# Kernel tuning notes

Hardware: AMD Instinct MI355X
Metric: run time of the kernel (lower is better)

## Reference

```python
import jax, jax.numpy as jnp
import numpy as np


def _resize_bilinear(x, h, w):
    # matches F.upsample(mode='bilinear', align_corners=False) (half-pixel centers)
    return jax.image.resize(x, (x.shape[0], x.shape[1], h, w), method='bilinear')


def _build_volume_2d(fl, fr, maxdisp):
    # fl, fr: [B,C,H,W] -> cost [B,D,H,W], D=maxdisp (stride=1)
    B, C, H, W = fl.shape
    d = jnp.arange(maxdisp)
    src = jnp.arange(W)[None, :] - d[:, None]          # [D,W]
    valid = (src >= 0).astype(fl.dtype)
    src_c = jnp.clip(src, 0, W - 1)
    fr_sh = fr[:, :, :, src_c] * valid                  # [B,C,H,D,W]; zeros where w<d
    cost = jnp.abs(fl[:, :, :, None, :] - fr_sh).sum(axis=1)  # [B,H,D,W]
    return jnp.transpose(cost, (0, 2, 1, 3))            # [B,D,H,W]


def _warp(fr, disp):
    # fr: [B,C,H,W]; disp: [B,K,H,W] horizontal disparity (sample at x - disp)
    # bilinear along W, zero padding (grid_sample semantics, align_corners=True grid)
    B, C, H, W = fr.shape
    xs = jnp.arange(W, dtype=fr.dtype)[None, None, None, :] - disp   # [B,K,H,W]
    x0 = jnp.floor(xs)
    w1 = xs - x0                                        # frac weight for right neighbor
    x0i = x0.astype(jnp.int32)
    x1i = x0i + 1
    v0 = ((x0i >= 0) & (x0i < W)).astype(fr.dtype)
    v1 = ((x1i >= 0) & (x1i < W)).astype(fr.dtype)
    x0c = jnp.clip(x0i, 0, W - 1)
    x1c = jnp.clip(x1i, 0, W - 1)

    def gather(idx):  # idx [B,K,H,W] -> [B,K,C,H,W]
        idxb = jnp.broadcast_to(idx[:, :, None, :, :], (B, idx.shape[1], C, H, W))
        return jnp.take_along_axis(fr[:, None], idxb, axis=-1)

    g0 = gather(x0c) * v0[:, :, None]
    g1 = gather(x1c) * v1[:, :, None]
    return g0 * (1.0 - w1)[:, :, None] + g1 * w1[:, :, None]   # [B,K,C,H,W]


def _build_volume_2d3(fl, fr, maxdisp, disp):
    # fl, fr: [B,C,H,W]; disp: [B,1,H,W] coarse disparity. K = 2*maxdisp-1 shifts.
    shifts = jnp.arange(-maxdisp + 1, maxdisp, dtype=fl.dtype)       # [K]
    bd = disp - shifts[None, :, None, None]                          # [B,K,H,W]
    warped = _warp(fr, bd)                                           # [B,K,C,H,W]
    return jnp.abs(fl[:, None] - warped).sum(axis=2)                 # [B,K,H,W]


def _regress(cost, start, end):
    # softmax(-cost) over disparity axis, weighted sum with disp values [start,end)
    p = jax.nn.softmax(-cost, axis=1)
    dvals = jnp.arange(start, end, dtype=cost.dtype)[None, :, None, None]
    return jnp.sum(p * dvals, axis=1, keepdims=True)                 # [B,1,H,W]


def setup_inputs() -> dict:
    key = jax.random.key(0)
    k = jax.random.split(key, 4)
    return {
        "feat_l0": jax.random.normal(k[0], (4, 32, 64, 128), dtype=jnp.float32),
        "feat_r0": jax.random.normal(k[1], (4, 32, 64, 128), dtype=jnp.float32),
        "feat_l1": jax.random.normal(k[2], (4, 32, 128, 256), dtype=jnp.float32),
        "feat_r1": jax.random.normal(k[3], (4, 32, 128, 256), dtype=jnp.float32),
        "img_h": 512,
        "img_w": 1024,
        "maxdisp0": 12,
        "maxdisp1": 3,
    }


def reference(feat_l0, feat_r0, feat_l1, feat_r1, img_h, img_w, maxdisp0, maxdisp1):
    H0 = feat_l0.shape[2]
    H1, W1 = feat_l1.shape[2], feat_l1.shape[3]

    cost0 = _build_volume_2d(feat_l0, feat_r0, maxdisp0)             # [B,D0,H0,W0]
    pred_low0 = _regress(cost0, 0, maxdisp0) * (img_h / H0)
    pred0 = _resize_bilinear(pred_low0, img_h, img_w)                # [B,1,img_h,img_w]

    # ---- scale 1: residual cost volume via warp around coarse disparity ----
    wflow = _resize_bilinear(pred0, H1, W1) * (H1 / img_h)           # [B,1,H1,W1]
    cost1 = _build_volume_2d3(feat_l1, feat_r1, maxdisp1, wflow)     # [B,2*D1-1,H1,W1]
    pred_low1 = _regress(cost1, -maxdisp1 + 1, maxdisp1) * (img_h / H1)
    pred1 = _resize_bilinear(pred_low1, img_h, img_w) + pred0

    return (pred0, pred1)
```

## Files before the change

### kernel.cpp

```cpp
#include <hip/hip_runtime.h>

#define NB 4
#define NC 32
#define H0 64
#define W0 128
#define D0 12
#define H1 128
#define W1 256
#define NK 5
#define IMH 512
#define IMW 1024

#define S0L 144
#define G0L 16
#define S1L 288
#define G1L 28

typedef __attribute__((address_space(3))) uint32_t as3_u32;
typedef const __attribute__((address_space(1))) uint32_t as1_u32;

__global__ __launch_bounds__(512) void k_main(
        const float* __restrict__ fl0, const float* __restrict__ fr0,
        const float* __restrict__ fl1, const float* __restrict__ fr1,
        float* __restrict__ pl0, float* __restrict__ pl1) {
    const int bk = blockIdx.x;
    const int b = bk >> 6, m = bk & 63;
    const int tid = threadIdx.x;
    const int wave = tid >> 6, lane = tid & 63;

    __shared__ float frs1[2][NC][S1L];
    __shared__ float frs0[3][NC][S0L];
    __shared__ float p0l[3][W0];
    __shared__ float ytmp[2][W0];
    __shared__ float wfl[2][W1];

#pragma unroll
    for (int j = 0; j < 8; ++j) {
        int idx = wave * 8 + j;
        int it = idx >> 5, c = idx & 31;
        const float* src = fr1 + ((size_t)(b * NC + c) * H1 + (2 * m + it)) * W1
                         + lane * 4;
        as3_u32* dst = (as3_u32*)&frs1[it][c][G1L];
        __builtin_amdgcn_global_load_lds((as1_u32*)src, dst, 16, 0, 0);
    }
    {
        int it = tid >> 8, c = (tid >> 3) & 31, u = tid & 7;
        int col = (u < 7) ? u * 4 : (G1L + W1);
        *(float4*)&frs1[it][c][col] = make_float4(0.f, 0.f, 0.f, 0.f);
    }

#pragma unroll
    for (int i = 0; i < 6; ++i) {
        int idx = i * 512 + tid;
        int rr = idx >> 10, rem = idx & 1023, c = rem >> 5, q = rem & 31;
        int row = min(max(m - 1 + rr, 0), H0 - 1);
        float4 v = *(const float4*)(fr0 + ((size_t)(b * NC + c) * H0 + row) * W0
                                    + q * 4);
        *(float4*)&frs0[rr][c][G0L + q * 4] = v;
    }
    if (tid < 384) {
        int rr = tid >> 7, c = (tid >> 2) & 31, u = tid & 3;
        *(float4*)&frs0[rr][c][u * 4] = make_float4(0.f, 0.f, 0.f, 0.f);
    }

    const int w0g = tid >> 2, g = tid & 3;
    float flv0[3][8];
#pragma unroll
    for (int rr = 0; rr < 3; ++rr) {
        int row = min(max(m - 1 + rr, 0), H0 - 1);
#pragma unroll
        for (int j = 0; j < 8; ++j)
            flv0[rr][j] = fl0[((size_t)(b * NC + 4 * j + g) * H0 + row) * W0 + w0g];
    }
    const int w1 = tid >> 1, hh = tid & 1;
    float flv1[2][16];
#pragma unroll
    for (int it = 0; it < 2; ++it)
#pragma unroll
        for (int j = 0; j < 16; ++j)
            flv1[it][j] = fl1[((size_t)(b * NC + 2 * j + hh) * H1 + 2 * m + it) * W1
                              + w1];
    __syncthreads();

#pragma unroll
    for (int rr = 0; rr < 3; ++rr) {
        float cost[D0];
#pragma unroll
        for (int d = 0; d < D0; ++d) cost[d] = 0.f;
#pragma unroll
        for (int j = 0; j < 8; ++j) {
            const float* sr = &frs0[rr][4 * j + g][G0L + w0g];
            float fv = flv0[rr][j];
#pragma unroll
            for (int d = 0; d < D0; ++d)
                cost[d] += fabsf(fv - sr[-d]);
        }
#pragma unroll
        for (int d = 0; d < D0; ++d) {
            cost[d] += __shfl_xor(cost[d], 1);
            cost[d] += __shfl_xor(cost[d], 2);
        }
        if (g == 0) {
            float mn = cost[0];
#pragma unroll
            for (int d = 1; d < D0; ++d) mn = fminf(mn, cost[d]);
            float s = 0.f, sd = 0.f;
#pragma unroll
            for (int d = 0; d < D0; ++d) {
                float e = expf(mn - cost[d]);
                s += e;
                sd += (float)d * e;
            }
            float val = 8.f * (sd / s);
            p0l[rr][w0g] = val;
            if (rr == 1)
                pl0[((size_t)b * H0 + m) * W0 + w0g] = val;
        }
    }
    __syncthreads();

    if (tid < 256) {
        int it = tid >> 7, col = tid & 127;
        int oy = 2 * m + it;
        float wy0, wy1, wy2;
        if (oy == 0)            { wy0 = 0.f;            wy1 = 27.625f / 28.f; wy2 = 0.375f / 28.f; }
        else if (oy == H1 - 1)  { wy0 = 0.375f / 28.f;  wy1 = 27.625f / 28.f; wy2 = 0.f; }
        else if (oy & 1)        { wy0 = 0.375f / 32.f;  wy1 = 23.25f / 32.f;  wy2 = 8.375f / 32.f; }
        else                    { wy0 = 8.375f / 32.f;  wy1 = 23.25f / 32.f;  wy2 = 0.375f / 32.f; }
        ytmp[it][col] = wy0 * p0l[0][col] + wy1 * p0l[1][col] + wy2 * p0l[2][col];
    }
    __syncthreads();
    {
        int it = tid >> 8, ox = tid & 255;
        int n = ox >> 1;
        int c0, c1, c2;
        float wx0, wx1, wx2;
        if (ox == 0) {
            c0 = 0; c1 = 0; c2 = 1;
            wx0 = 0.f; wx1 = 27.625f / 28.f; wx2 = 0.375f / 28.f;
        } else if (ox == W1 - 1) {
            c0 = W0 - 2; c1 = W0 - 1; c2 = W0 - 1;
            wx0 = 0.375f / 28.f; wx1 = 27.625f / 28.f; wx2 = 0.f;
        } else {
            c0 = max(n - 1, 0); c1 = n; c2 = min(n + 1, W0 - 1);
            if (ox & 1) { wx0 = 0.375f / 32.f; wx1 = 23.25f / 32.f; wx2 = 8.375f / 32.f; }
            else        { wx0 = 8.375f / 32.f; wx1 = 23.25f / 32.f; wx2 = 0.375f / 32.f; }
        }
        wfl[it][ox] = 0.25f * (wx0 * ytmp[it][c0] + wx1 * ytmp[it][c1]
                             + wx2 * ytmp[it][c2]);
    }
    __syncthreads();

#pragma unroll
    for (int it = 0; it < 2; ++it) {
        float disp = wfl[it][w1];
        float xs = (float)w1 - disp;
        float xbf = floorf(xs);
        float f = xs - xbf;
        int xb = (int)xbf;
        const float* sr = &frs1[it][0][G1L + xb - 2];

        float cost[NK];
#pragma unroll
        for (int k = 0; k < NK; ++k) cost[k] = 0.f;
#pragma unroll
        for (int j = 0; j < 16; ++j) {
            const float* row = sr + (2 * j + hh) * S1L;
            float g0 = row[0], g1 = row[1], g2 = row[2];
            float g3 = row[3], g4 = row[4], g5 = row[5];
            float fv = flv1[it][j];
            cost[0] += fabsf(fv - (g0 + f * (g1 - g0)));
            cost[1] += fabsf(fv - (g1 + f * (g2 - g1)));
            cost[2] += fabsf(fv - (g2 + f * (g3 - g2)));
            cost[3] += fabsf(fv - (g3 + f * (g4 - g3)));
            cost[4] += fabsf(fv - (g5 * f + g4 * (1.f - f)));
        }
#pragma unroll
        for (int k = 0; k < NK; ++k) cost[k] += __shfl_xor(cost[k], 1);
        if (hh == 0) {
            float mn = cost[0];
#pragma unroll
            for (int k = 1; k < NK; ++k) mn = fminf(mn, cost[k]);
            float s = 0.f, sd = 0.f;
#pragma unroll
            for (int k = 0; k < NK; ++k) {
                float e = expf(mn - cost[k]);
                s += e;
                sd += (float)(k - 2) * e;
            }
            pl1[((size_t)b * H1 + 2 * m + it) * W1 + w1] = 4.f * (sd / s);
        }
    }
}

__global__ __launch_bounds__(256, 4) void k_final(const float* __restrict__ pl0,
                                                  const float* __restrict__ pl1,
                                                  float* __restrict__ out) {
    const int blk = blockIdx.x;
    const int b = blk >> 9, y = blk & (IMH - 1);
    const int tid = threadIdx.x;
    __shared__ float a0[W0];
    __shared__ float a1[W1];

    const float* p0b = pl0 + (size_t)b * H0 * W0;
    const float* p1b = pl1 + (size_t)b * H1 * W1;

    float sy0 = (y + 0.5f) * 0.125f - 0.5f;
    float y0f = floorf(sy0);
    float fy0 = sy0 - y0f;
    int r0 = (int)y0f;
    int r0c = min(max(r0, 0), H0 - 1), r1c = min(max(r0 + 1, 0), H0 - 1);

    float sy1 = (y + 0.5f) * 0.25f - 0.5f;
    float y1f = floorf(sy1);
    float fy1 = sy1 - y1f;
    int s0 = (int)y1f;
    int s0c = min(max(s0, 0), H1 - 1), s1c = min(max(s0 + 1, 0), H1 - 1);

    if (tid < W0) {
        float u = p0b[r0c * W0 + tid], v = p0b[r1c * W0 + tid];
        a0[tid] = u + fy0 * (v - u);
    }
    {
        float u = p1b[s0c * W1 + tid], v = p1b[s1c * W1 + tid];
        a1[tid] = u + fy1 * (v - u);
    }
    __syncthreads();

    float v0[4], v1[4];
#pragma unroll
    for (int i = 0; i < 4; ++i) {
        int x = tid * 4 + i;
        float sx0 = (x + 0.5f) * 0.125f - 0.5f;
        float x0f = floorf(sx0);
        float fx0 = sx0 - x0f;
        int c0 = (int)x0f;
        int c0c = min(max(c0, 0), W0 - 1), c1c = min(max(c0 + 1, 0), W0 - 1);
        float p0 = a0[c0c] + fx0 * (a0[c1c] - a0[c0c]);

        float sx1 = (x + 0.5f) * 0.25f - 0.5f;
        float x1f = floorf(sx1);
        float fx1 = sx1 - x1f;
        int d0 = (int)x1f;
        int d0c = min(max(d0, 0), W1 - 1), d1c = min(max(d0 + 1, 0), W1 - 1);
        float p1 = a1[d0c] + fx1 * (a1[d1c] - a1[d0c]);

        v0[i] = p0;
        v1[i] = p1 + p0;
    }
    const size_t NPXQ = (size_t)NB * IMH * IMW / 4;
    size_t t = (size_t)blk * 256 + tid;
    ((float4*)out)[t] = make_float4(v0[0], v0[1], v0[2], v0[3]);
    ((float4*)out)[NPXQ + t] = make_float4(v1[0], v1[1], v1[2], v1[3]);
}

extern "C" void kernel_launch(void* const* d_in, const int* in_sizes, int n_in,
                              void* d_out, int out_size, void* d_ws, size_t ws_size,
                              hipStream_t stream) {
    const float* fl0 = (const float*)d_in[0];
    const float* fr0 = (const float*)d_in[1];
    const float* fl1 = (const float*)d_in[2];
    const float* fr1 = (const float*)d_in[3];
    float* out = (float*)d_out;

    float* ws = (float*)d_ws;
    float* pl0 = ws;
    float* pl1 = ws + 32768;

    k_main<<<NB * H0, 512, 0, stream>>>(fl0, fr0, fl1, fr1, pl0, pl1);
    k_final<<<NB * IMH, 256, 0, stream>>>(pl0, pl1, out);
}
```

Baseline: 30.45 us.

## Split main kernel blocks into horizontal halves to double grid parallelism

Each block now handles half the width of a row pair, so the grid doubles from 256 to 512 blocks and more CUs are occupied on a large GPU. Shared tiles shrink to half-width plus halo, loads use bounds-checked float4 instead of async global_load_lds, and per-thread channel splits widen (8-way and 4-way), which adds shuffle reductions. A halo column of the coarse prediction is recomputed redundantly by 8 threads, and the halo rows of the scale-0 cost are now computed by twice as many blocks.

```diff
diff --git a/kernel.cpp b/kernel.cpp
--- a/kernel.cpp
+++ b/kernel.cpp
@@ -11,75 +11,87 @@
 #define IMH 512
 #define IMW 1024
 
-#define S0L 144
-#define G0L 16
-#define S1L 288
-#define G1L 28
-
-typedef __attribute__((address_space(3))) uint32_t as3_u32;
-typedef const __attribute__((address_space(1))) uint32_t as1_u32;
-
-__global__ __launch_bounds__(512) void k_main(
+#define S0L 88
+#define S1L 168
+
+__global__ __launch_bounds__(512, 4) void k_main(
         const float* __restrict__ fl0, const float* __restrict__ fr0,
         const float* __restrict__ fl1, const float* __restrict__ fr1,
         float* __restrict__ pl0, float* __restrict__ pl1) {
     const int bk = blockIdx.x;
-    const int b = bk >> 6, m = bk & 63;
+    const int xh = bk & 1;
+    const int mb = bk >> 1;
+    const int b = mb >> 6, m = mb & 63;
     const int tid = threadIdx.x;
-    const int wave = tid >> 6, lane = tid & 63;
-
+
+    __shared__ float frs0[3][NC][S0L];
     __shared__ float frs1[2][NC][S1L];
-    __shared__ float frs0[3][NC][S0L];
-    __shared__ float p0l[3][W0];
-    __shared__ float ytmp[2][W0];
-    __shared__ float wfl[2][W1];
-
-#pragma unroll
-    for (int j = 0; j < 8; ++j) {
-        int idx = wave * 8 + j;
-        int it = idx >> 5, c = idx & 31;
-        const float* src = fr1 + ((size_t)(b * NC + c) * H1 + (2 * m + it)) * W1
-                         + lane * 4;
-        as3_u32* dst = (as3_u32*)&frs1[it][c][G1L];
-        __builtin_amdgcn_global_load_lds((as1_u32*)src, dst, 16, 0, 0);
-    }
-    {
-        int it = tid >> 8, c = (tid >> 3) & 31, u = tid & 7;
-        int col = (u < 7) ? u * 4 : (G1L + W1);
-        *(float4*)&frs1[it][c][col] = make_float4(0.f, 0.f, 0.f, 0.f);
+    __shared__ float p0l[3][65];
+    __shared__ float ytmp[2][65];
+    __shared__ float wfl[2][128];
+
+    const int colp = xh * 63;
+    const int s0c0 = xh * 64 - 16;
+    const int s1c0 = xh * 128 - 28;
+
+#pragma unroll
+    for (int i = 0; i < 5; ++i) {
+        int idx = i * 512 + tid;
+        if (idx < 2112) {
+            int rr = idx / 704, rem = idx - rr * 704;
+            int c = rem / 22, q = rem - c * 22;
+            int row = min(max(m - 1 + rr, 0), H0 - 1);
+            int colg = s0c0 + 4 * q;
+            float4 v = make_float4(0.f, 0.f, 0.f, 0.f);
+            if (colg >= 0 && colg <= W0 - 4)
+                v = *(const float4*)(fr0 + ((size_t)(b * NC + c) * H0 + row) * W0 + colg);
+            *(float4*)&frs0[rr][c][4 * q] = v;
+        }
+    }
+
+    const int wl = tid >> 3, g = tid & 7;
+    float flv0[3][4];
+#pragma unroll
+    for (int rr = 0; rr < 3; ++rr) {
+        int row = min(max(m - 1 + rr, 0), H0 - 1);
+#pragma unroll
+        for (int j = 0; j < 4; ++j)
+            flv0[rr][j] = fl0[((size_t)(b * NC + 8 * j + g) * H0 + row) * W0 + colp + wl];
+    }
+    float flv0e[3][4];
+    if (tid < 8) {
+#pragma unroll
+        for (int rr = 0; rr < 3; ++rr) {
+            int row = min(max(m - 1 + rr, 0), H0 - 1);
+#pragma unroll
+            for (int j = 0; j < 4; ++j)
+                flv0e[rr][j] = fl0[((size_t)(b * NC + 8 * j + g) * H0 + row) * W0 + colp + 64];
+        }
     }
 
 #pragma unroll
     for (int i = 0; i < 6; ++i) {
         int idx = i * 512 + tid;
-        int rr = idx >> 10, rem = idx & 1023, c = rem >> 5, q = rem & 31;
-        int row = min(max(m - 1 + rr, 0), H0 - 1);
-        float4 v = *(const float4*)(fr0 + ((size_t)(b * NC + c) * H0 + row) * W0
-                                    + q * 4);
-        *(float4*)&frs0[rr][c][G0L + q * 4] = v;
-    }
-    if (tid < 384) {
-        int rr = tid >> 7, c = (tid >> 2) & 31, u = tid & 3;
-        *(float4*)&frs0[rr][c][u * 4] = make_float4(0.f, 0.f, 0.f, 0.f);
-    }
-
-    const int w0g = tid >> 2, g = tid & 3;
-    float flv0[3][8];
-#pragma unroll
-    for (int rr = 0; rr < 3; ++rr) {
-        int row = min(max(m - 1 + rr, 0), H0 - 1);
+        if (idx < 2688) {
+            int it = idx / 1344, rem = idx - it * 1344;
+            int c = rem / 42, q = rem - c * 42;
+            int colg = s1c0 + 4 * q;
+            float4 v = make_float4(0.f, 0.f, 0.f, 0.f);
+            if (colg >= 0 && colg <= W1 - 4)
+                v = *(const float4*)(fr1 + ((size_t)(b * NC + c) * H1 + 2 * m + it) * W1 + colg);
+            *(float4*)&frs1[it][c][4 * q] = v;
+        }
+    }
+
+    const int oxl = tid >> 2, sub = tid & 3;
+    const int w1 = xh * 128 + oxl;
+    float flv1[2][8];
+#pragma unroll
+    for (int it = 0; it < 2; ++it)
 #pragma unroll
         for (int j = 0; j < 8; ++j)
-            flv0[rr][j] = fl0[((size_t)(b * NC + 4 * j + g) * H0 + row) * W0 + w0g];
-    }
-    const int w1 = tid >> 1, hh = tid & 1;
-    float flv1[2][16];
-#pragma unroll
-    for (int it = 0; it < 2; ++it)
-#pragma unroll
-        for (int j = 0; j < 16; ++j)
-            flv1[it][j] = fl1[((size_t)(b * NC + 2 * j + hh) * H1 + 2 * m + it) * W1
-                              + w1];
+            flv1[it][j] = fl1[((size_t)(b * NC + 4 * j + sub) * H1 + 2 * m + it) * W1 + w1];
+
     __syncthreads();
 
 #pragma unroll
@@ -88,8 +100,8 @@
 #pragma unroll
         for (int d = 0; d < D0; ++d) cost[d] = 0.f;
 #pragma unroll
-        for (int j = 0; j < 8; ++j) {
-            const float* sr = &frs0[rr][4 * j + g][G0L + w0g];
+        for (int j = 0; j < 4; ++j) {
+            const float* sr = &frs0[rr][8 * j + g][16 - xh + wl];
             float fv = flv0[rr][j];
 #pragma unroll
             for (int d = 0; d < D0; ++d)
@@ -99,6 +111,7 @@
         for (int d = 0; d < D0; ++d) {
             cost[d] += __shfl_xor(cost[d], 1);
             cost[d] += __shfl_xor(cost[d], 2);
+            cost[d] += __shfl_xor(cost[d], 4);
         }
         if (g == 0) {
             float mn = cost[0];
@@ -112,60 +125,100 @@
                 sd += (float)d * e;
             }
             float val = 8.f * (sd / s);
-            p0l[rr][w0g] = val;
+            p0l[rr][wl] = val;
             if (rr == 1)
-                pl0[((size_t)b * H0 + m) * W0 + w0g] = val;
-        }
-    }
-    __syncthreads();
-
-    if (tid < 256) {
-        int it = tid >> 7, col = tid & 127;
+                pl0[((size_t)b * H0 + m) * W0 + colp + wl] = val;
+        }
+    }
+    if (tid < 8) {
+#pragma unroll
+        for (int rr = 0; rr < 3; ++rr) {
+            float cost[D0];
+#pragma unroll
+            for (int d = 0; d < D0; ++d) cost[d] = 0.f;
+#pragma unroll
+            for (int j = 0; j < 4; ++j) {
+                const float* sr = &frs0[rr][8 * j + g][16 - xh + 64];
+                float fv = flv0e[rr][j];
+#pragma unroll
+                for (int d = 0; d < D0; ++d)
+                    cost[d] += fabsf(fv - sr[-d]);
+            }
+#pragma unroll
+            for (int d = 0; d < D0; ++d) {
+                cost[d] += __shfl_xor(cost[d], 1);
+                cost[d] += __shfl_xor(cost[d], 2);
+                cost[d] += __shfl_xor(cost[d], 4);
+            }
+            if (g == 0) {
+                float mn = cost[0];
+#pragma unroll
+                for (int d = 1; d < D0; ++d) mn = fminf(mn, cost[d]);
+                float s = 0.f, sd = 0.f;
+#pragma unroll
+                for (int d = 0; d < D0; ++d) {
+                    float e = expf(mn - cost[d]);
+                    s += e;
+                    sd += (float)d * e;
+                }
+                float val = 8.f * (sd / s);
+                p0l[rr][64] = val;
+                if (rr == 1)
+                    pl0[((size_t)b * H0 + m) * W0 + colp + 64] = val;
+            }
+        }
+    }
+    __syncthreads();
+
+    if (tid < 256 && (tid & 127) < 65) {
+        int it = tid >> 7, q = tid & 127;
         int oy = 2 * m + it;
         float wy0, wy1, wy2;
-        if (oy == 0)            { wy0 = 0.f;            wy1 = 27.625f / 28.f; wy2 = 0.375f / 28.f; }
-        else if (oy == H1 - 1)  { wy0 = 0.375f / 28.f;  wy1 = 27.625f / 28.f; wy2 = 0.f; }
-        else if (oy & 1)        { wy0 = 0.375f / 32.f;  wy1 = 23.25f / 32.f;  wy2 = 8.375f / 32.f; }
-        else                    { wy0 = 8.375f / 32.f;  wy1 = 23.25f / 32.f;  wy2 = 0.375f / 32.f; }
-        ytmp[it][col] = wy0 * p0l[0][col] + wy1 * p0l[1][col] + wy2 * p0l[2][col];
-    }
-    __syncthreads();
-    {
-        int it = tid >> 8, ox = tid & 255;
+        if (oy == 0)           { wy0 = 0.f;           wy1 = 27.625f / 28.f; wy2 = 0.375f / 28.f; }
+        else if (oy == H1 - 1) { wy0 = 0.375f / 28.f; wy1 = 27.625f / 28.f; wy2 = 0.f; }
+        else if (oy & 1)       { wy0 = 0.375f / 32.f; wy1 = 23.25f / 32.f;  wy2 = 8.375f / 32.f; }
+        else                   { wy0 = 8.375f / 32.f; wy1 = 23.25f / 32.f;  wy2 = 0.375f / 32.f; }
+        ytmp[it][q] = wy0 * p0l[0][q] + wy1 * p0l[1][q] + wy2 * p0l[2][q];
+    }
+    __syncthreads();
+
+    if (tid < 256) {
+        int it = tid >> 7, ol = tid & 127;
+        int ox = xh * 128 + ol;
         int n = ox >> 1;
-        int c0, c1, c2;
+        int c0l, c1l, c2l;
         float wx0, wx1, wx2;
         if (ox == 0) {
-            c0 = 0; c1 = 0; c2 = 1;
+            c0l = 0; c1l = 0; c2l = 1;
             wx0 = 0.f; wx1 = 27.625f / 28.f; wx2 = 0.375f / 28.f;
         } else if (ox == W1 - 1) {
-            c0 = W0 - 2; c1 = W0 - 1; c2 = W0 - 1;
+            c0l = 63; c1l = 64; c2l = 64;
             wx0 = 0.375f / 28.f; wx1 = 27.625f / 28.f; wx2 = 0.f;
         } else {
-            c0 = max(n - 1, 0); c1 = n; c2 = min(n + 1, W0 - 1);
+            c0l = max(n - 1, 0) - colp; c1l = n - colp; c2l = min(n + 1, W0 - 1) - colp;
             if (ox & 1) { wx0 = 0.375f / 32.f; wx1 = 23.25f / 32.f; wx2 = 8.375f / 32.f; }
             else        { wx0 = 8.375f / 32.f; wx1 = 23.25f / 32.f; wx2 = 0.375f / 32.f; }
         }
-        wfl[it][ox] = 0.25f * (wx0 * ytmp[it][c0] + wx1 * ytmp[it][c1]
-                             + wx2 * ytmp[it][c2]);
+        wfl[it][ol] = 0.25f * (wx0 * ytmp[it][c0l] + wx1 * ytmp[it][c1l]
+                             + wx2 * ytmp[it][c2l]);
     }
     __syncthreads();
 
 #pragma unroll
     for (int it = 0; it < 2; ++it) {
-        float disp = wfl[it][w1];
+        float disp = wfl[it][oxl];
         float xs = (float)w1 - disp;
         float xbf = floorf(xs);
         float f = xs - xbf;
         int xb = (int)xbf;
-        const float* sr = &frs1[it][0][G1L + xb - 2];
+        const float* sr = &frs1[it][0][xb - xh * 128 + 26];
 
         float cost[NK];
 #pragma unroll
         for (int k = 0; k < NK; ++k) cost[k] = 0.f;
 #pragma unroll
-        for (int j = 0; j < 16; ++j) {
-            const float* row = sr + (2 * j + hh) * S1L;
+        for (int j = 0; j < 8; ++j) {
+            const float* row = sr + (4 * j + sub) * S1L;
             float g0 = row[0], g1 = row[1], g2 = row[2];
             float g3 = row[3], g4 = row[4], g5 = row[5];
             float fv = flv1[it][j];
@@ -176,8 +229,11 @@
             cost[4] += fabsf(fv - (g5 * f + g4 * (1.f - f)));
         }
 #pragma unroll
-        for (int k = 0; k < NK; ++k) cost[k] += __shfl_xor(cost[k], 1);
-        if (hh == 0) {
+        for (int k = 0; k < NK; ++k) {
+            cost[k] += __shfl_xor(cost[k], 1);
+            cost[k] += __shfl_xor(cost[k], 2);
+        }
+        if (sub == 0) {
             float mn = cost[0];
 #pragma unroll
             for (int k = 1; k < NK; ++k) mn = fminf(mn, cost[k]);
@@ -267,6 +323,6 @@
     float* pl0 = ws;
     float* pl1 = ws + 32768;
 
-    k_main<<<NB * H0, 512, 0, stream>>>(fl0, fr0, fl1, fr1, pl0, pl1);
+    k_main<<<NB * H0 * 2, 512, 0, stream>>>(fl0, fr0, fl1, fr1, pl0, pl1);
     k_final<<<NB * IMH, 256, 0, stream>>>(pl0, pl1, out);
 }
```

Result: slower. 36.64 us (+20.3%).
